# Performance work log

Measured on AMD Instinct MI355X. Metric: run time of the kernel, lower is better.

The kernel has to match this reference:

```python
import jax, jax.numpy as jnp
import numpy as np

LN_EPS = 1e-5
NRM_EPS = 1e-12


def layernorm(x, w, b):
    mu = x.mean(-1, keepdims=True)
    var = ((x - mu) ** 2).mean(-1, keepdims=True)
    return (x - mu) * jax.lax.rsqrt(var + LN_EPS) * w + b


def cdist(x, y):
    # Euclidean pairwise distance over trailing (N, C): (..., N, C) x (..., M, C) -> (..., N, M)
    x2 = (x * x).sum(-1)
    y2 = (y * y).sum(-1)
    xy = jnp.einsum('...ic,...jc->...ij', x, y)
    return jnp.sqrt(jnp.maximum(x2[..., :, None] + y2[..., None, :] - 2.0 * xy, NRM_EPS))


def l2norm_last(x):
    n = jnp.sqrt((x * x).sum(-1, keepdims=True))
    return x / jnp.maximum(n, NRM_EPS)


def attn_qcs_sd(anchor, positive, neg1, neg2, k, alpha):
    # anchor/positive: (B,N,C); neg1/neg2: (2,B,N,C)
    # torch.tensor(neg) in the original detaches neg1/neg2 from autograd
    neg1 = jax.lax.stop_gradient(neg1)
    neg2 = jax.lax.stop_gradient(neg2)
    k = k + 1.0
    S_p = cdist(positive, anchor)           # (B,N,N)
    S_p = S_p - S_p.min()
    S_p = S_p.max() - S_p
    S_a = l2norm_last(S_p).sum(1)           # (B,N)
    S_p1 = l2norm_last(jnp.swapaxes(S_p, 1, 2)).sum(1)  # (B,N)

    def proc(D):  # (B,N,N) -> (B,N)
        D = D - D.min()
        return l2norm_last(D).sum(1)

    def pair(neg, tgt):  # neg (2,B,N,C), tgt (B,N,C)
        D = cdist(neg, jnp.broadcast_to(tgt[None], neg.shape))  # (2,B,N,N)
        return proc(D[0]), proc(D[1])

    d11, d12 = pair(neg1, anchor)
    d21, d22 = pair(neg2, anchor)
    map1 = S_a + k * ((d11 + d12) / 2 * alpha + (1 - alpha) * ((d21 + d22) / 2))
    d11, d12 = pair(neg1, positive)
    d21, d22 = pair(neg2, positive)
    map2 = S_p1 + k * ((d11 + d12) / 2 * alpha + (1 - alpha) * ((d21 + d22) / 2))
    return map1[..., None], map2[..., None]  # (B,N,1) each


def setup_inputs() -> dict:
    key = jax.random.key(0)
    B, N, C = 8, 1024, 768
    ks = jax.random.split(key, 12)
    s = 1.0 / np.sqrt(C)
    sh = 1.0 / np.sqrt(4 * C)
    return {
        'anchor': jax.random.normal(ks[0], (B, N, C), jnp.float32),
        'positive': jax.random.normal(ks[1], (B, N, C), jnp.float32),
        'neg1': jax.random.normal(ks[2], (2, B, N, C), jnp.float32),
        'neg2': jax.random.normal(ks[3], (2, B, N, C), jnp.float32),
        'norm1_w': jnp.ones((C,), jnp.float32),
        'norm1_b': jnp.zeros((C,), jnp.float32),
        'norm2_w': jnp.ones((C,), jnp.float32),
        'norm2_b': jnp.zeros((C,), jnp.float32),
        'proj_W': jax.random.uniform(ks[4], (C, 2 * C), jnp.float32, -s, s),
        'proj_b': jax.random.uniform(ks[5], (2 * C,), jnp.float32, -s, s),
        'fc1_W': jax.random.uniform(ks[6], (C, 4 * C), jnp.float32, -s, s),
        'fc1_b': jax.random.uniform(ks[7], (4 * C,), jnp.float32, -s, s),
        'fc2_W': jax.random.uniform(ks[8], (4 * C, C), jnp.float32, -sh, sh),
        'fc2_b': jax.random.uniform(ks[9], (C,), jnp.float32, -sh, sh),
        'theta': jnp.float32(0.0),
        'alpha': jnp.float32(0.0),
    }


def reference(anchor, positive, neg1, neg2, norm1_w, norm1_b, norm2_w, norm2_b,
              proj_W, proj_b, fc1_W, fc1_b, fc2_W, fc2_b, theta, alpha):
    def projsplit(x):
        y = x @ proj_W + proj_b
        C = x.shape[-1]
        return y[..., :C], y[..., C:]  # qk, v

    anc = layernorm(anchor, norm1_w, norm1_b)
    pos = layernorm(positive, norm1_w, norm1_b)
    n1 = layernorm(neg1, norm1_w, norm1_b)   # (2,B,N,C)
    n2 = layernorm(neg2, norm1_w, norm1_b)
    qk_x, v_x = projsplit(anc)
    qk_p, v_p = projsplit(pos)
    qk_n1, v_n1 = projsplit(n1)
    qk_n2, v_n2 = projsplit(n2)

    k = jnp.tanh(theta)
    al = jax.nn.sigmoid(alpha)

    a_a, a_p = attn_qcs_sd(qk_x, qk_p, qk_n1, qk_n2, k, al)
    n1_a, n1_p = attn_qcs_sd(qk_n1[0], qk_n1[1], jnp.stack([qk_x, qk_p]), qk_n2, k, al)
    n2_a, n2_p = attn_qcs_sd(qk_n2[0], qk_n2[1], jnp.stack([qk_x, qk_p]), qk_n1, k, al)

    anc_o = a_a * v_x + anc
    pos_o = a_p * v_p + pos
    neg1_o = jnp.stack([n1_a * v_n1[0] * n1[0], n1_p * v_n1[1] * n1[1]])
    neg2_o = jnp.stack([n2_a * v_n2[0] * n2[0], n2_p * v_n2[1] * n2[1]])

    def block(x):
        h = layernorm(x, norm2_w, norm2_b)
        h = jax.nn.gelu(h @ fc1_W + fc1_b, approximate=False) @ fc2_W + fc2_b
        return h + x

    return block(anc_o), block(pos_o), block(neg1_o), block(neg2_o)
```

## Files before the change

kernel.cpp:

```cpp
#include <hip/hip_runtime.h>
#include <hip/hip_bf16.h>


typedef short bshort8 __attribute__((ext_vector_type(8)));
typedef unsigned short u16x8 __attribute__((ext_vector_type(8)));
typedef float f32x4  __attribute__((ext_vector_type(4)));

#define AS1 __attribute__((address_space(1)))
#define AS3 __attribute__((address_space(3)))

#define B_   8
#define N_   1024
#define C_   768
#define MT   8192
#define M6   49152

#define OFF_QKNORM   0ull
#define OFF_MAPS     196608ull
#define OFF_STATS    393216ull
#define OFF_WBUF     2359296ull
#define OFF_MM       3342336ull
#define MEMSET_BYTES 3342464ull
#define OFF_WTPROJ   3342592ull
#define OFF_WTFC1    5701888ull
#define OFF_WTFC2    10420480ull
#define OFF_LNBF     15139072ull
#define OFF_QKBF     90636544ull
#define OFF_XHBF     OFF_QKBF
#define OFF_VBF      166134016ull
#define OFF_DBUF     241631488ull
#define OFF_H1BF     OFF_DBUF

__constant__ int cSU[15] = {1,3,5, 2,3,4,5, 2,3,4,5, 4,5,4,5};
__constant__ int cSV[15] = {0,2,4, 0,0,0,0, 1,1,1,1, 2,2,3,3};
__constant__ int cTA[15] = {0,0,0, 1,1,2,2, 1,1,2,2, 2,2,2,2};
__constant__ int cTB[15] = {0,0,0, 1,1,1,1, 1,1,1,1, 2,2,2,2};

__device__ __forceinline__ void gll16(const void* g, void* l) {
    __builtin_amdgcn_global_load_lds((const AS1 unsigned int*)g,
                                     (AS3 unsigned int*)l, 16, 0, 0);
}
__device__ __forceinline__ unsigned short f2bu(float v) {
    __hip_bfloat16 h = __float2bfloat16(v);
    return *reinterpret_cast<unsigned short*>(&h);
}
__device__ __forceinline__ float bu2f(unsigned short u) {
    __hip_bfloat16 h;
    *reinterpret_cast<unsigned short*>(&h) = u;
    return __bfloat162float(h);
}

__device__ __forceinline__ void gemm_core(const __hip_bfloat16* __restrict__ A,
                                          const __hip_bfloat16* __restrict__ Bt,
                                          int lda, int ldb, int kIters,
                                          char* smem, f32x4 acc[4][4])
{
    const int tid  = threadIdx.x;
    const int w    = tid >> 6;
    const int L    = tid & 63;
    const int srow = L >> 2;
    const int schunk = (L & 3) ^ ((L >> 3) & 3);

    const char* ga0 = (const char*)(A  + (size_t)(32*w      + srow) * lda + schunk*8);
    const char* ga1 = (const char*)(A  + (size_t)(32*w + 16 + srow) * lda + schunk*8);
    const char* gb0 = (const char*)(Bt + (size_t)(32*w      + srow) * ldb + schunk*8);
    const char* gb1 = (const char*)(Bt + (size_t)(32*w + 16 + srow) * ldb + schunk*8);
    const int la0 = (32*w)*64;
    const int la1 = (32*w+16)*64;
    const int lb0 = 8192 + (32*w)*64;
    const int lb1 = 8192 + (32*w+16)*64;

    const int m = L & 15, q = L >> 4;
    const int wr = (w >> 1) * 64, wc = (w & 1) * 64;
    const int roff = 16 * (q ^ ((m >> 1) & 3));
    int ra[4], rb[4];
#pragma unroll
    for (int s = 0; s < 4; ++s) {
        ra[s] = (wr + 16*s + m) * 64 + roff;
        rb[s] = 8192 + (wc + 16*s + m) * 64 + roff;
    }
    f32x4 z = {0.f, 0.f, 0.f, 0.f};
#pragma unroll
    for (int s = 0; s < 4; ++s)
#pragma unroll
        for (int t = 0; t < 4; ++t) acc[s][t] = z;

    char* b0 = smem;
    char* b1 = smem + 16384;

    gll16(ga0, b0 + la0); gll16(ga1, b0 + la1);
    gll16(gb0, b0 + lb0); gll16(gb1, b0 + lb1);
    ga0 += 64; ga1 += 64; gb0 += 64; gb1 += 64;

    auto step = [&](char* cur, char* nxt, bool last) {
        __syncthreads();
        if (!last) {
            gll16(ga0, nxt + la0); gll16(ga1, nxt + la1);
            gll16(gb0, nxt + lb0); gll16(gb1, nxt + lb1);
            ga0 += 64; ga1 += 64; gb0 += 64; gb1 += 64;
        }
        bshort8 af[4], bfr[4];
#pragma unroll
        for (int s = 0; s < 4; ++s) af[s]  = *(const bshort8*)(cur + ra[s]);
#pragma unroll
        for (int t = 0; t < 4; ++t) bfr[t] = *(const bshort8*)(cur + rb[t]);
#pragma unroll
        for (int s = 0; s < 4; ++s)
#pragma unroll
            for (int t = 0; t < 4; ++t)
                acc[s][t] = __builtin_amdgcn_mfma_f32_16x16x32_bf16(af[s], bfr[t], acc[s][t], 0, 0, 0);
    };

    for (int kt = 0; kt < kIters; kt += 2) {
        step(b0, b1, false);
        step(b1, b0, kt + 2 >= kIters);
    }
}

__global__ __launch_bounds__(256) void transpose_conv(const float* __restrict__ in,
                                                      __hip_bfloat16* __restrict__ out,
                                                      int R, int C)
{
    __shared__ float tile[32][33];
    int bx = blockIdx.x * 32, by = blockIdx.y * 32;
    int tx = threadIdx.x, ty = threadIdx.y;
#pragma unroll
    for (int i = 0; i < 32; i += 8)
        tile[ty + i][tx] = in[(size_t)(by + ty + i) * C + bx + tx];
    __syncthreads();
#pragma unroll
    for (int i = 0; i < 32; i += 8)
        out[(size_t)(bx + ty + i) * R + by + tx] = __float2bfloat16(tile[tx][ty + i]);
}

__global__ void init_mm(unsigned int* mm)
{
    int i = threadIdx.x;
    if (i < 15) { mm[i] = 0x7f800000u; mm[15 + i] = 0u; }
}

__global__ __launch_bounds__(256) void ln1_kernel(const float* __restrict__ anchor,
                                                  const float* __restrict__ positive,
                                                  const float* __restrict__ neg1,
                                                  const float* __restrict__ neg2,
                                                  const float* __restrict__ w1,
                                                  const float* __restrict__ b1,
                                                  __hip_bfloat16* __restrict__ lnbf)
{
    int w = threadIdx.x >> 6, L = threadIdx.x & 63;
    int r = blockIdx.x * 4 + w;
    int t = r >> 13, within = r & 8191;
    const float* src;
    if      (t == 0) src = anchor   + (size_t)within * C_;
    else if (t == 1) src = positive + (size_t)within * C_;
    else if (t <  4) src = neg1 + ((size_t)(t - 2) * MT + within) * C_;
    else             src = neg2 + ((size_t)(t - 4) * MT + within) * C_;
    float4 x[3]; float s = 0.f, sq = 0.f;
#pragma unroll
    for (int j = 0; j < 3; ++j) {
        x[j] = *(const float4*)(src + 4 * L + 256 * j);
        s  += x[j].x + x[j].y + x[j].z + x[j].w;
        sq += x[j].x*x[j].x + x[j].y*x[j].y + x[j].z*x[j].z + x[j].w*x[j].w;
    }
#pragma unroll
    for (int o = 1; o < 64; o <<= 1) { s += __shfl_xor(s, o, 64); sq += __shfl_xor(sq, o, 64); }
    float mu  = s * (1.f / 768.f);
    float var = sq * (1.f / 768.f) - mu * mu;
    float rs  = rsqrtf(var + 1e-5f);
    __hip_bfloat16* dst = lnbf + (size_t)r * C_;
#pragma unroll
    for (int j = 0; j < 3; ++j) {
        int c = 4 * L + 256 * j;
        float4 wv = *(const float4*)(w1 + c);
        float4 bv = *(const float4*)(b1 + c);
        ushort4 o;
        o.x = f2bu((x[j].x - mu) * rs * wv.x + bv.x);
        o.y = f2bu((x[j].y - mu) * rs * wv.y + bv.y);
        o.z = f2bu((x[j].z - mu) * rs * wv.z + bv.z);
        o.w = f2bu((x[j].w - mu) * rs * wv.w + bv.w);
        *(ushort4*)(dst + c) = o;
    }
}

__global__ __launch_bounds__(256) void gemm_proj(const __hip_bfloat16* __restrict__ A,
                                                 const __hip_bfloat16* __restrict__ Wt,
                                                 const float* __restrict__ bias,
                                                 __hip_bfloat16* __restrict__ qkbf,
                                                 __hip_bfloat16* __restrict__ vbf,
                                                 float* __restrict__ qknorm)
{
    __shared__ __align__(16) char smem[32768];
    f32x4 acc[4][4];
    gemm_core(A + (size_t)blockIdx.y * 128 * C_, Wt + (size_t)blockIdx.x * 128 * C_,
              C_, C_, 24, smem, acc);
    int tid = threadIdx.x, w = tid >> 6, L = tid & 63, m = L & 15, q = L >> 4;
    int rowBase = blockIdx.y * 128 + (w >> 1) * 64;
    int colBase = blockIdx.x * 128 + (w & 1) * 64;
    bool isQK = (blockIdx.x < 6);
#pragma unroll
    for (int s = 0; s < 4; ++s) {
#pragma unroll
        for (int r = 0; r < 4; ++r) {
            int row = rowBase + 16 * s + 4 * q + r;
            float sqsum = 0.f;
#pragma unroll
            for (int t = 0; t < 4; ++t) {
                int col = colBase + 16 * t + m;
                float val = acc[s][t][r] + bias[col];
                if (isQK) {
                    qkbf[(size_t)row * C_ + col] = __float2bfloat16(val);
                    sqsum += val * val;
                } else {
                    vbf[(size_t)row * C_ + (col - C_)] = __float2bfloat16(val);
                }
            }
            if (isQK) {
#pragma unroll
                for (int o = 1; o < 16; o <<= 1) sqsum += __shfl_xor(sqsum, o, 64);
                if (m == 0) atomicAdd(qknorm + row, sqsum);
            }
        }
    }
}

__global__ __launch_bounds__(256) void gram_kernel(const __hip_bfloat16* __restrict__ qkbf,
                                                   const float* __restrict__ qknorm,
                                                   __hip_bfloat16* __restrict__ Dbuf,
                                                   float* __restrict__ stats,
                                                   unsigned int* __restrict__ mm,
                                                   int sb)
{
    __shared__ __align__(16) char smem[32768];
    int z = blockIdx.z, slab = sb + z, b = blockIdx.y;
    int ti = blockIdx.x >> 3, tj = blockIdx.x & 7;
    int u = cSU[slab], v = cSV[slab];

    const __hip_bfloat16* Ab = qkbf + (size_t)(u * MT + b * N_ + ti * 128) * C_;
    const __hip_bfloat16* Bb = qkbf + (size_t)(v * MT + b * N_ + tj * 128) * C_;
    f32x4 acc[4][4];
    gemm_core(Ab, Bb, C_, C_, 24, smem, acc);

    int tid = threadIdx.x, w = tid >> 6, L = tid & 63, m = L & 15, q = L >> 4;
    int rowBase = ti * 128 + (w >> 1) * 64;
    int colBase = tj * 128 + (w & 1) * 64;
    const float* nu = qknorm + u * MT + b * N_;
    const float* nv = qknorm + v * MT + b * N_;
    float nbv[4];
#pragma unroll
    for (int t = 0; t < 4; ++t) nbv[t] = nv[colBase + 16 * t + m];

    __hip_bfloat16* Drow = Dbuf + (size_t)z * 8388608ull + ((size_t)b << 20);
    float* rs1 = stats + (size_t)slab * 32768;
    float* rs2 = rs1 + 8192;
    float* cs1 = rs1 + 16384;
    float* cs2 = rs1 + 24576;

    float dmin = 3.0e38f, dmax = 0.f;
    float col1[4] = {0.f,0.f,0.f,0.f}, col2[4] = {0.f,0.f,0.f,0.f};
#pragma unroll
    for (int s = 0; s < 4; ++s) {
#pragma unroll
        for (int r = 0; r < 4; ++r) {
            int row = rowBase + 16 * s + 4 * q + r;
            float na = nu[row];
            float h1 = 0.f, h2 = 0.f;
#pragma unroll
            for (int t = 0; t < 4; ++t) {
                float dval = sqrtf(fmaxf(na + nbv[t] - 2.f * acc[s][t][r], 1e-12f));
                Drow[(size_t)row * N_ + colBase + 16 * t + m] = __float2bfloat16(dval);
                h1 += dval; h2 += dval * dval;
                col1[t] += dval; col2[t] += dval * dval;
                dmin = fminf(dmin, dval); dmax = fmaxf(dmax, dval);
            }
#pragma unroll
            for (int o = 1; o < 16; o <<= 1) { h1 += __shfl_xor(h1, o, 64); h2 += __shfl_xor(h2, o, 64); }
            if (m == 0) { atomicAdd(rs1 + b * N_ + row, h1); atomicAdd(rs2 + b * N_ + row, h2); }
        }
    }
#pragma unroll
    for (int t = 0; t < 4; ++t) {
        float c1 = col1[t], c2 = col2[t];
        c1 += __shfl_xor(c1, 16, 64); c1 += __shfl_xor(c1, 32, 64);
        c2 += __shfl_xor(c2, 16, 64); c2 += __shfl_xor(c2, 32, 64);
        if (q == 0) {
            int col = colBase + 16 * t + m;
            atomicAdd(cs1 + b * N_ + col, c1);
            atomicAdd(cs2 + b * N_ + col, c2);
        }
    }
#pragma unroll
    for (int o = 1; o < 64; o <<= 1) {
        dmin = fminf(dmin, __shfl_xor(dmin, o, 64));
        dmax = fmaxf(dmax, __shfl_xor(dmax, o, 64));
    }
    if (L == 0) {
        atomicMin(mm + slab, __float_as_uint(dmin));
        atomicMax(mm + 15 + slab, __float_as_uint(dmax));
    }
}

__global__ __launch_bounds__(256) void weights_kernel(const float* __restrict__ stats,
                                                      const unsigned int* __restrict__ mm,
                                                      float* __restrict__ wbuf,
                                                      float* __restrict__ maps,
                                                      const float* __restrict__ theta,
                                                      const float* __restrict__ alpha,
                                                      int sb)
{
    int job = blockIdx.x, b = blockIdx.y;
    int slab = sb + (job >> 1);
    int useB = job & 1;
    const float* s1 = stats + (size_t)slab * 32768 + useB * 16384;
    const float* s2 = s1 + 8192;
    int type = useB ? cTB[slab] : cTA[slab];
    int dst  = useB ? cSU[slab] : cSV[slab];
    float off = (type == 0) ? __uint_as_float(mm[15 + slab]) : __uint_as_float(mm[slab]);
    float k  = tanhf(theta[0]) + 1.0f;
    float al = 1.0f / (1.0f + expf(-alpha[0]));
    float cf = (type == 0) ? -1.0f : ((type == 1) ? 0.5f * k * al : 0.5f * k * (1.0f - al));
    float* wout = wbuf + (size_t)slab * 16384 + useB * 8192 + b * N_;

    float sumw = 0.f;
    for (int i = threadIdx.x; i < N_; i += 256) {
        float a1 = s1[b * N_ + i], a2 = s2[b * N_ + i];
        float nrm2  = fmaxf(a2 - 2.f * off * a1 + (float)N_ * off * off, 0.f);
        float denom = fmaxf(sqrtf(nrm2), 1e-12f);
        float wv = cf / denom;
        wout[i] = wv;
        sumw += wv;
    }
    int w = threadIdx.x >> 6, L = threadIdx.x & 63;
#pragma unroll
    for (int o = 1; o < 64; o <<= 1) sumw += __shfl_xor(sumw, o, 64);
    __shared__ float red[4];
    if (L == 0) red[w] = sumw;
    __syncthreads();
    float tot = red[0] + red[1] + red[2] + red[3];
    float Cb = -off * tot;
    for (int j = threadIdx.x; j < N_; j += 256)
        atomicAdd(maps + (size_t)dst * MT + b * N_ + j, Cb);
}

__global__ __launch_bounds__(256) void wsum_kernel(const __hip_bfloat16* __restrict__ Dbuf,
                                                   const float* __restrict__ wbuf,
                                                   float* __restrict__ maps,
                                                   int sb)
{
    int z = blockIdx.z, slab = sb + z, b = blockIdx.y;
    int ti = blockIdx.x >> 3, tj = blockIdx.x & 7;
    int u = cSU[slab], v = cSV[slab];
    const __hip_bfloat16* D = Dbuf + (size_t)z * 8388608ull + ((size_t)b << 20)
                              + (size_t)ti * 128 * N_ + tj * 128;
    const float* wr = wbuf + (size_t)slab * 16384 + b * N_ + ti * 128;
    const float* wc = wbuf + (size_t)slab * 16384 + 8192 + b * N_ + tj * 128;

    __shared__ float swr[128], swc[128], scol[128];
    if (threadIdx.x < 128) { swr[threadIdx.x] = wr[threadIdx.x]; scol[threadIdx.x] = 0.f; }
    else                   { swc[threadIdx.x - 128] = wc[threadIdx.x - 128]; }
    __syncthreads();

    int tx = threadIdx.x & 15, ty = threadIdx.x >> 4;
    float wce[8];
#pragma unroll
    for (int e = 0; e < 8; ++e) wce[e] = swc[8 * tx + e];
    float c[8] = {0.f,0.f,0.f,0.f,0.f,0.f,0.f,0.f};
#pragma unroll 2
    for (int rr = 0; rr < 8; ++rr) {
        int row = ty + rr * 16;
        u16x8 dv8 = *(const u16x8*)(D + (size_t)row * N_ + 8 * tx);
        float wrow = swr[row];
        float rd = 0.f;
#pragma unroll
        for (int e = 0; e < 8; ++e) {
            float d = bu2f(dv8[e]);
            c[e] += wrow * d;
            rd += wce[e] * d;
        }
#pragma unroll
        for (int o = 1; o < 16; o <<= 1) rd += __shfl_xor(rd, o, 64);
        if (tx == 0) atomicAdd(maps + (size_t)u * MT + b * N_ + ti * 128 + row, rd);
    }
#pragma unroll
    for (int e = 0; e < 8; ++e) atomicAdd(&scol[8 * tx + e], c[e]);
    __syncthreads();
    if (threadIdx.x < 128)
        atomicAdd(maps + (size_t)v * MT + b * N_ + tj * 128 + threadIdx.x, scol[threadIdx.x]);
}

__global__ __launch_bounds__(256) void combine_ln2(const float* __restrict__ maps,
                                                   const __hip_bfloat16* __restrict__ vbf,
                                                   const __hip_bfloat16* __restrict__ lnbf,
                                                   const float* __restrict__ w2,
                                                   const float* __restrict__ b2,
                                                   float* __restrict__ dout,
                                                   __hip_bfloat16* __restrict__ xhbf)
{
    int w = threadIdx.x >> 6, L = threadIdx.x & 63;
    int r = blockIdx.x * 4 + w;
    int t = r >> 13;
    float mv = maps[r];
    const __hip_bfloat16* vp = vbf + (size_t)r * C_;
    const __hip_bfloat16* lp = lnbf + (size_t)r * C_;
    float x[12]; float s = 0.f, sq = 0.f;
#pragma unroll
    for (int j = 0; j < 3; ++j) {
        int c = 4 * L + 256 * j;
        ushort4 vv = *(const ushort4*)(vp + c);
        ushort4 ll = *(const ushort4*)(lp + c);
        float xv[4];
        xv[0] = (t < 2) ? (mv * bu2f(vv.x) + bu2f(ll.x)) : (mv * bu2f(vv.x) * bu2f(ll.x));
        xv[1] = (t < 2) ? (mv * bu2f(vv.y) + bu2f(ll.y)) : (mv * bu2f(vv.y) * bu2f(ll.y));
        xv[2] = (t < 2) ? (mv * bu2f(vv.z) + bu2f(ll.z)) : (mv * bu2f(vv.z) * bu2f(ll.z));
        xv[3] = (t < 2) ? (mv * bu2f(vv.w) + bu2f(ll.w)) : (mv * bu2f(vv.w) * bu2f(ll.w));
        float4 xo = {xv[0], xv[1], xv[2], xv[3]};
        *(float4*)(dout + (size_t)r * C_ + c) = xo;
#pragma unroll
        for (int e = 0; e < 4; ++e) { x[4*j+e] = xv[e]; s += xv[e]; sq += xv[e]*xv[e]; }
    }
#pragma unroll
    for (int o = 1; o < 64; o <<= 1) { s += __shfl_xor(s, o, 64); sq += __shfl_xor(sq, o, 64); }
    float mu  = s * (1.f / 768.f);
    float var = sq * (1.f / 768.f) - mu * mu;
    float rs  = rsqrtf(var + 1e-5f);
    __hip_bfloat16* dst = xhbf + (size_t)r * C_;
#pragma unroll
    for (int j = 0; j < 3; ++j) {
        int c = 4 * L + 256 * j;
        float4 wv = *(const float4*)(w2 + c);
        float4 bv = *(const float4*)(b2 + c);
        ushort4 o;
        o.x = f2bu((x[4*j+0] - mu) * rs * wv.x + bv.x);
        o.y = f2bu((x[4*j+1] - mu) * rs * wv.y + bv.y);
        o.z = f2bu((x[4*j+2] - mu) * rs * wv.z + bv.z);
        o.w = f2bu((x[4*j+3] - mu) * rs * wv.w + bv.w);
        *(ushort4*)(dst + c) = o;
    }
}

__global__ __launch_bounds__(256) void gemm_ffn1(const __hip_bfloat16* __restrict__ A,
                                                 const __hip_bfloat16* __restrict__ Wt,
                                                 const float* __restrict__ bias,
                                                 __hip_bfloat16* __restrict__ h1)
{
    __shared__ __align__(16) char smem[32768];
    f32x4 acc[4][4];
    gemm_core(A + (size_t)blockIdx.y * 128 * C_, Wt + (size_t)blockIdx.x * 128 * C_,
              C_, C_, 24, smem, acc);
    int tid = threadIdx.x, w = tid >> 6, L = tid & 63, m = L & 15, q = L >> 4;
    int rowBase = blockIdx.y * 128 + (w >> 1) * 64;
    int colBase = blockIdx.x * 128 + (w & 1) * 64;
#pragma unroll
    for (int s = 0; s < 4; ++s)
#pragma unroll
        for (int r = 0; r < 4; ++r) {
            int row = rowBase + 16 * s + 4 * q + r;
#pragma unroll
            for (int t = 0; t < 4; ++t) {
                int col = colBase + 16 * t + m;
                float val = acc[s][t][r] + bias[col];
                float ge  = 0.5f * val * (1.0f + erff(val * 0.70710678118654752f));
                h1[(size_t)row * 3072 + col] = __float2bfloat16(ge);
            }
        }
}

__global__ __launch_bounds__(256) void gemm_ffn2(const __hip_bfloat16* __restrict__ A,
                                                 const __hip_bfloat16* __restrict__ Wt,
                                                 const float* __restrict__ bias,
                                                 float* __restrict__ out)
{
    __shared__ __align__(16) char smem[32768];
    f32x4 acc[4][4];
    gemm_core(A + (size_t)blockIdx.y * 128 * 3072, Wt + (size_t)blockIdx.x * 128 * 3072,
              3072, 3072, 96, smem, acc);
    int tid = threadIdx.x, w = tid >> 6, L = tid & 63, m = L & 15, q = L >> 4;
    int rowBase = blockIdx.y * 128 + (w >> 1) * 64;
    int colBase = blockIdx.x * 128 + (w & 1) * 64;
#pragma unroll
    for (int s = 0; s < 4; ++s)
#pragma unroll
        for (int r = 0; r < 4; ++r) {
            int row = rowBase + 16 * s + 4 * q + r;
#pragma unroll
            for (int t = 0; t < 4; ++t) {
                int col = colBase + 16 * t + m;
                size_t idx = (size_t)row * C_ + col;
                out[idx] = out[idx] + acc[s][t][r] + bias[col];
            }
        }
}

extern "C" void kernel_launch(void* const* d_in, const int* in_sizes, int n_in,
                              void* d_out, int out_size, void* d_ws, size_t ws_size,
                              hipStream_t stream)
{
    (void)in_sizes; (void)n_in; (void)out_size; (void)ws_size;
    const float* anchor   = (const float*)d_in[0];
    const float* positive = (const float*)d_in[1];
    const float* neg1     = (const float*)d_in[2];
    const float* neg2     = (const float*)d_in[3];
    const float* n1w      = (const float*)d_in[4];
    const float* n1b      = (const float*)d_in[5];
    const float* n2w      = (const float*)d_in[6];
    const float* n2b      = (const float*)d_in[7];
    const float* projW    = (const float*)d_in[8];
    const float* projb    = (const float*)d_in[9];
    const float* fc1W     = (const float*)d_in[10];
    const float* fc1b     = (const float*)d_in[11];
    const float* fc2W     = (const float*)d_in[12];
    const float* fc2b     = (const float*)d_in[13];
    const float* theta    = (const float*)d_in[14];
    const float* alpha    = (const float*)d_in[15];
    float* dout = (float*)d_out;

    char* ws = (char*)d_ws;
    float*          qknorm = (float*)(ws + OFF_QKNORM);
    float*          maps   = (float*)(ws + OFF_MAPS);
    float*          stats  = (float*)(ws + OFF_STATS);
    float*          wbuf   = (float*)(ws + OFF_WBUF);
    unsigned int*   mm     = (unsigned int*)(ws + OFF_MM);
    __hip_bfloat16* WtProj = (__hip_bfloat16*)(ws + OFF_WTPROJ);
    __hip_bfloat16* WtFc1  = (__hip_bfloat16*)(ws + OFF_WTFC1);
    __hip_bfloat16* WtFc2  = (__hip_bfloat16*)(ws + OFF_WTFC2);
    __hip_bfloat16* lnbf   = (__hip_bfloat16*)(ws + OFF_LNBF);
    __hip_bfloat16* qkbf   = (__hip_bfloat16*)(ws + OFF_QKBF);
    __hip_bfloat16* xhbf   = (__hip_bfloat16*)(ws + OFF_XHBF);
    __hip_bfloat16* vbf    = (__hip_bfloat16*)(ws + OFF_VBF);
    __hip_bfloat16* Dbuf   = (__hip_bfloat16*)(ws + OFF_DBUF);
    __hip_bfloat16* h1bf   = (__hip_bfloat16*)(ws + OFF_H1BF);

    hipMemsetAsync(ws, 0, MEMSET_BYTES, stream);
    init_mm<<<1, 64, 0, stream>>>(mm);

    transpose_conv<<<dim3(48, 24), dim3(32, 8), 0, stream>>>(projW, WtProj, 768, 1536);
    transpose_conv<<<dim3(96, 24), dim3(32, 8), 0, stream>>>(fc1W,  WtFc1,  768, 3072);
    transpose_conv<<<dim3(24, 96), dim3(32, 8), 0, stream>>>(fc2W,  WtFc2,  3072, 768);

    ln1_kernel<<<12288, 256, 0, stream>>>(anchor, positive, neg1, neg2, n1w, n1b, lnbf);

    gemm_proj<<<dim3(12, 384), 256, 0, stream>>>(lnbf, WtProj, projb, qkbf, vbf, qknorm);

    for (int g = 0; g < 2; ++g) {
        int sb = g * 8;
        int ns = g ? 7 : 8;
        gram_kernel<<<dim3(64, 8, ns), 256, 0, stream>>>(qkbf, qknorm, Dbuf, stats, mm, sb);
        weights_kernel<<<dim3(2 * ns, 8), 256, 0, stream>>>(stats, mm, wbuf, maps, theta, alpha, sb);
        wsum_kernel<<<dim3(64, 8, ns), 256, 0, stream>>>(Dbuf, wbuf, maps, sb);
    }

    combine_ln2<<<12288, 256, 0, stream>>>(maps, vbf, lnbf, n2w, n2b, dout, xhbf);

    for (int ch = 0; ch < 2; ++ch) {
        size_t ro = (size_t)ch * 24576;
        gemm_ffn1<<<dim3(24, 192), 256, 0, stream>>>(xhbf + ro * C_, WtFc1, fc1b, h1bf);
        gemm_ffn2<<<dim3(6, 192), 256, 0, stream>>>(h1bf, WtFc2, fc2b, dout + ro * C_);
    }
}
```

Measured before the change: 2.145 ms.

## Store distance tiles in fragment-native layout and swizzle GEMM workgroups across XCDs

```diff
diff --git a/kernel.cpp b/kernel.cpp
--- a/kernel.cpp
+++ b/kernel.cpp
@@ -49,6 +49,9 @@
     *reinterpret_cast<unsigned short*>(&h) = u;
     return __bfloat162float(h);
 }
+__device__ __forceinline__ int xcd_swz(int flat, int nwg) {
+    return (flat & 7) * (nwg >> 3) + (flat >> 3);
+}
 
 __device__ __forceinline__ void gemm_core(const __hip_bfloat16* __restrict__ A,
                                           const __hip_bfloat16* __restrict__ Bt,
@@ -190,13 +193,16 @@
                                                  float* __restrict__ qknorm)
 {
     __shared__ __align__(16) char smem[32768];
+    int flat = blockIdx.x + 12 * blockIdx.y;
+    int sf   = xcd_swz(flat, 12 * 384);
+    int bx = sf % 12, by = sf / 12;
     f32x4 acc[4][4];
-    gemm_core(A + (size_t)blockIdx.y * 128 * C_, Wt + (size_t)blockIdx.x * 128 * C_,
+    gemm_core(A + (size_t)by * 128 * C_, Wt + (size_t)bx * 128 * C_,
               C_, C_, 24, smem, acc);
     int tid = threadIdx.x, w = tid >> 6, L = tid & 63, m = L & 15, q = L >> 4;
-    int rowBase = blockIdx.y * 128 + (w >> 1) * 64;
-    int colBase = blockIdx.x * 128 + (w & 1) * 64;
-    bool isQK = (blockIdx.x < 6);
+    int rowBase = by * 128 + (w >> 1) * 64;
+    int colBase = bx * 128 + (w & 1) * 64;
+    bool isQK = (bx < 6);
 #pragma unroll
     for (int s = 0; s < 4; ++s) {
 #pragma unroll
@@ -231,8 +237,14 @@
                                                    int sb)
 {
     __shared__ __align__(16) char smem[32768];
-    int z = blockIdx.z, slab = sb + z, b = blockIdx.y;
-    int ti = blockIdx.x >> 3, tj = blockIdx.x & 7;
+    int flat = blockIdx.x + 64 * blockIdx.y + 512 * blockIdx.z;
+    int nwg  = 512 * gridDim.z;
+    int sf   = xcd_swz(flat, nwg);
+    int tile = sf & 63;
+    int b    = (sf >> 6) & 7;
+    int z    = sf >> 9;
+    int slab = sb + z;
+    int ti = tile >> 3, tj = tile & 7;
     int u = cSU[slab], v = cSV[slab];
 
     const __hip_bfloat16* Ab = qkbf + (size_t)(u * MT + b * N_ + ti * 128) * C_;
@@ -249,7 +261,8 @@
 #pragma unroll
     for (int t = 0; t < 4; ++t) nbv[t] = nv[colBase + 16 * t + m];
 
-    __hip_bfloat16* Drow = Dbuf + (size_t)z * 8388608ull + ((size_t)b << 20);
+    unsigned short* Dc = (unsigned short*)Dbuf + (size_t)z * 8388608ull
+                         + ((size_t)b << 20) + (size_t)tile * 16384 + w * 4096;
     float* rs1 = stats + (size_t)slab * 32768;
     float* rs2 = rs1 + 8192;
     float* cs1 = rs1 + 16384;
@@ -259,22 +272,40 @@
     float col1[4] = {0.f,0.f,0.f,0.f}, col2[4] = {0.f,0.f,0.f,0.f};
 #pragma unroll
     for (int s = 0; s < 4; ++s) {
+        float na[4];
+#pragma unroll
+        for (int r = 0; r < 4; ++r) na[r] = nu[rowBase + 16 * s + 4 * q + r];
+        float dv[4][4];
+        float h1v[4] = {0.f,0.f,0.f,0.f}, h2v[4] = {0.f,0.f,0.f,0.f};
+#pragma unroll
+        for (int t = 0; t < 4; ++t) {
+#pragma unroll
+            for (int r = 0; r < 4; ++r) {
+                float d = sqrtf(fmaxf(na[r] + nbv[t] - 2.f * acc[s][t][r], 1e-12f));
+                dv[t][r] = d;
+                h1v[r] += d; h2v[r] += d * d;
+                col1[t] += d; col2[t] += d * d;
+                dmin = fminf(dmin, d); dmax = fmaxf(dmax, d);
+            }
+        }
+#pragma unroll
+        for (int tp = 0; tp < 2; ++tp) {
+            u16x8 pk;
+#pragma unroll
+            for (int e = 0; e < 8; ++e)
+                pk[e] = f2bu(dv[2 * tp + (e >> 2)][e & 3]);
+            *(u16x8*)(Dc + (s * 2 + tp) * 512 + m * 32 + q * 8) = pk;
+        }
 #pragma unroll
         for (int r = 0; r < 4; ++r) {
-            int row = rowBase + 16 * s + 4 * q + r;
-            float na = nu[row];
-            float h1 = 0.f, h2 = 0.f;
-#pragma unroll
-            for (int t = 0; t < 4; ++t) {
-                float dval = sqrtf(fmaxf(na + nbv[t] - 2.f * acc[s][t][r], 1e-12f));
-                Drow[(size_t)row * N_ + colBase + 16 * t + m] = __float2bfloat16(dval);
-                h1 += dval; h2 += dval * dval;
-                col1[t] += dval; col2[t] += dval * dval;
-                dmin = fminf(dmin, dval); dmax = fmaxf(dmax, dval);
+            float h1 = h1v[r], h2 = h2v[r];
+#pragma unroll
+            for (int o = 1; o < 16; o <<= 1) { h1 += __shfl_xor(h1, o, 64); h2 += __shfl_xor(h2, o, 64); }
+            if (m == 0) {
+                int row = rowBase + 16 * s + 4 * q + r;
+                atomicAdd(rs1 + b * N_ + row, h1);
+                atomicAdd(rs2 + b * N_ + row, h2);
             }
-#pragma unroll
-            for (int o = 1; o < 16; o <<= 1) { h1 += __shfl_xor(h1, o, 64); h2 += __shfl_xor(h2, o, 64); }
-            if (m == 0) { atomicAdd(rs1 + b * N_ + row, h1); atomicAdd(rs2 + b * N_ + row, h2); }
         }
     }
 #pragma unroll
@@ -347,44 +378,68 @@
                                                    int sb)
 {
     int z = blockIdx.z, slab = sb + z, b = blockIdx.y;
-    int ti = blockIdx.x >> 3, tj = blockIdx.x & 7;
+    int tile = blockIdx.x;
+    int ti = tile >> 3, tj = tile & 7;
     int u = cSU[slab], v = cSV[slab];
-    const __hip_bfloat16* D = Dbuf + (size_t)z * 8388608ull + ((size_t)b << 20)
-                              + (size_t)ti * 128 * N_ + tj * 128;
+    int tid = threadIdx.x, w = tid >> 6, L = tid & 63, m = L & 15, q = L >> 4;
+    const unsigned short* Dc = (const unsigned short*)Dbuf + (size_t)z * 8388608ull
+                               + ((size_t)b << 20) + (size_t)tile * 16384 + w * 4096;
     const float* wr = wbuf + (size_t)slab * 16384 + b * N_ + ti * 128;
     const float* wc = wbuf + (size_t)slab * 16384 + 8192 + b * N_ + tj * 128;
 
-    __shared__ float swr[128], swc[128], scol[128];
-    if (threadIdx.x < 128) { swr[threadIdx.x] = wr[threadIdx.x]; scol[threadIdx.x] = 0.f; }
-    else                   { swc[threadIdx.x - 128] = wc[threadIdx.x - 128]; }
+    __shared__ float swr[128], swc[128];
+    if (threadIdx.x < 128) swr[threadIdx.x] = wr[threadIdx.x];
+    else                   swc[threadIdx.x - 128] = wc[threadIdx.x - 128];
     __syncthreads();
 
-    int tx = threadIdx.x & 15, ty = threadIdx.x >> 4;
-    float wce[8];
-#pragma unroll
-    for (int e = 0; e < 8; ++e) wce[e] = swc[8 * tx + e];
-    float c[8] = {0.f,0.f,0.f,0.f,0.f,0.f,0.f,0.f};
-#pragma unroll 2
-    for (int rr = 0; rr < 8; ++rr) {
-        int row = ty + rr * 16;
-        u16x8 dv8 = *(const u16x8*)(D + (size_t)row * N_ + 8 * tx);
-        float wrow = swr[row];
-        float rd = 0.f;
-#pragma unroll
-        for (int e = 0; e < 8; ++e) {
-            float d = bu2f(dv8[e]);
-            c[e] += wrow * d;
-            rd += wce[e] * d;
-        }
-#pragma unroll
-        for (int o = 1; o < 16; o <<= 1) rd += __shfl_xor(rd, o, 64);
-        if (tx == 0) atomicAdd(maps + (size_t)u * MT + b * N_ + ti * 128 + row, rd);
-    }
-#pragma unroll
-    for (int e = 0; e < 8; ++e) atomicAdd(&scol[8 * tx + e], c[e]);
-    __syncthreads();
-    if (threadIdx.x < 128)
-        atomicAdd(maps + (size_t)v * MT + b * N_ + tj * 128 + threadIdx.x, scol[threadIdx.x]);
+    int wrbase = (w >> 1) * 64, wcbase = (w & 1) * 64;
+    float wc1[4];
+#pragma unroll
+    for (int t = 0; t < 4; ++t) wc1[t] = swc[wcbase + 16 * t + m];
+    float wr4[4][4];
+#pragma unroll
+    for (int s = 0; s < 4; ++s)
+#pragma unroll
+        for (int r = 0; r < 4; ++r) wr4[s][r] = swr[wrbase + 16 * s + 4 * q + r];
+
+    float rowacc[4][4];
+#pragma unroll
+    for (int s = 0; s < 4; ++s)
+#pragma unroll
+        for (int r = 0; r < 4; ++r) rowacc[s][r] = 0.f;
+    float colacc[4] = {0.f,0.f,0.f,0.f};
+
+#pragma unroll
+    for (int s = 0; s < 4; ++s) {
+#pragma unroll
+        for (int tp = 0; tp < 2; ++tp) {
+            u16x8 d8 = *(const u16x8*)(Dc + (s * 2 + tp) * 512 + m * 32 + q * 8);
+#pragma unroll
+            for (int e = 0; e < 8; ++e) {
+                int t = 2 * tp + (e >> 2), r = e & 3;
+                float d = bu2f(d8[e]);
+                rowacc[s][r] += wc1[t] * d;
+                colacc[t]    += wr4[s][r] * d;
+            }
+        }
+    }
+#pragma unroll
+    for (int s = 0; s < 4; ++s)
+#pragma unroll
+        for (int r = 0; r < 4; ++r) {
+            float h = rowacc[s][r];
+#pragma unroll
+            for (int o = 1; o < 16; o <<= 1) h += __shfl_xor(h, o, 64);
+            if (m == 0)
+                atomicAdd(maps + (size_t)u * MT + b * N_ + ti * 128 + wrbase + 16 * s + 4 * q + r, h);
+        }
+#pragma unroll
+    for (int t = 0; t < 4; ++t) {
+        float c = colacc[t];
+        c += __shfl_xor(c, 16, 64); c += __shfl_xor(c, 32, 64);
+        if (q == 0)
+            atomicAdd(maps + (size_t)v * MT + b * N_ + tj * 128 + wcbase + 16 * t + m, c);
+    }
 }
 
 __global__ __launch_bounds__(256) void combine_ln2(const float* __restrict__ maps,
@@ -443,12 +498,15 @@
                                                  __hip_bfloat16* __restrict__ h1)
 {
     __shared__ __align__(16) char smem[32768];
+    int flat = blockIdx.x + 24 * blockIdx.y;
+    int sf   = xcd_swz(flat, 24 * 192);
+    int bx = sf % 24, by = sf / 24;
     f32x4 acc[4][4];
-    gemm_core(A + (size_t)blockIdx.y * 128 * C_, Wt + (size_t)blockIdx.x * 128 * C_,
+    gemm_core(A + (size_t)by * 128 * C_, Wt + (size_t)bx * 128 * C_,
               C_, C_, 24, smem, acc);
     int tid = threadIdx.x, w = tid >> 6, L = tid & 63, m = L & 15, q = L >> 4;
-    int rowBase = blockIdx.y * 128 + (w >> 1) * 64;
-    int colBase = blockIdx.x * 128 + (w & 1) * 64;
+    int rowBase = by * 128 + (w >> 1) * 64;
+    int colBase = bx * 128 + (w & 1) * 64;
 #pragma unroll
     for (int s = 0; s < 4; ++s)
 #pragma unroll
@@ -470,12 +528,15 @@
                                                  float* __restrict__ out)
 {
     __shared__ __align__(16) char smem[32768];
+    int flat = blockIdx.x + 6 * blockIdx.y;
+    int sf   = xcd_swz(flat, 6 * 192);
+    int bx = sf % 6, by = sf / 6;
     f32x4 acc[4][4];
-    gemm_core(A + (size_t)blockIdx.y * 128 * 3072, Wt + (size_t)blockIdx.x * 128 * 3072,
+    gemm_core(A + (size_t)by * 128 * 3072, Wt + (size_t)bx * 128 * 3072,
               3072, 3072, 96, smem, acc);
     int tid = threadIdx.x, w = tid >> 6, L = tid & 63, m = L & 15, q = L >> 4;
-    int rowBase = blockIdx.y * 128 + (w >> 1) * 64;
-    int colBase = blockIdx.x * 128 + (w & 1) * 64;
+    int rowBase = by * 128 + (w >> 1) * 64;
+    int colBase = bx * 128 + (w & 1) * 64;
 #pragma unroll
     for (int s = 0; s < 4; ++s)
 #pragma unroll
```

After: 1.971 ms. -8.1%, faster.
